# Performance work log

Measured on AMD Instinct MI355X. Metric: run time of the kernel, lower is better.

Reference implementation:

```python
import math
import jax, jax.numpy as jnp
import numpy as np

B, FEAT, H, W = 4, 256, 48, 48
NH = 8
PE = 10            # pe_dim -> 3*PE = 30 positional channels
DK = FEAT // NH    # 32
DV = FEAT // NH    # 32
SCALE = 2.0 * math.pi
TEMPERATURE = 10000.0
BN_EPS = 1e-5


def pos_en_sine(h, w, num_pos_feats=PE):
    """3-axis sine positional encoding (y, x, and a constant 'o' axis) -> [3*PE, h, w]."""
    eps = 1e-6
    ones = jnp.ones((h, w), jnp.float32)
    y_embed = jnp.cumsum(ones, axis=0)
    x_embed = jnp.cumsum(ones, axis=1)
    y_embed = y_embed / (y_embed[-1:, :] + eps) * SCALE
    x_embed = x_embed / (x_embed[:, -1:] + eps) * SCALE
    o_embed = ones * SCALE  # third axis, constant when no explicit pos is given
    dim_t = jnp.arange(num_pos_feats, dtype=jnp.float32)
    dim_t = TEMPERATURE ** (2.0 * jnp.floor(dim_t / 2.0) / num_pos_feats)

    def enc(e):  # e: [h, w] -> [h, w, PE] interleaved sin/cos
        p = e[..., None] / dim_t
        return jnp.stack([jnp.sin(p[..., 0::2]), jnp.cos(p[..., 1::2])], axis=-1).reshape(h, w, num_pos_feats)

    pe = jnp.concatenate([enc(y_embed), enc(x_embed), enc(o_embed)], axis=-1)  # [h, w, 3*PE]
    return jnp.transpose(pe, (2, 0, 1))  # [3*PE, h, w]


def conv1x1(w, x):  # w: [out_c, in_c], x: [b, in_c, h, w]
    return jnp.einsum('oc,bchw->bohw', w, x)


def setup_inputs() -> dict:
    key = jax.random.key(0)
    ks = jax.random.split(key, 16)
    s = 0.02
    return {
        'q': jax.random.normal(ks[0], (B, FEAT, H, W), jnp.float32),
        'k': jax.random.normal(ks[1], (B, FEAT, H, W), jnp.float32),
        'v': jax.random.normal(ks[2], (B, FEAT, H, W), jnp.float32),
        'wq': jax.random.normal(ks[3], (NH * DK, FEAT + 3 * PE), jnp.float32) * s,
        'wk': jax.random.normal(ks[4], (NH * DK, FEAT + 3 * PE), jnp.float32) * s,
        'wv': jax.random.normal(ks[5], (NH * DV, FEAT), jnp.float32) * s,
        'wfc': jax.random.normal(ks[6], (FEAT, NH * DV), jnp.float32) * s,
        'w1': jax.random.normal(ks[7], (FEAT, FEAT), jnp.float32) * s,
        'b1': jnp.zeros((FEAT,), jnp.float32),
        'w2': jax.random.normal(ks[8], (FEAT, FEAT), jnp.float32) * s,
        'b2': jnp.zeros((FEAT,), jnp.float32),
        'gamma': jnp.ones((FEAT,), jnp.float32),
        'beta': jnp.zeros((FEAT,), jnp.float32),
    }


def reference(q, k, v, wq, wk, wv, wfc, w1, b1, w2, b2, gamma, beta):
    b, c, h, w = q.shape
    n = h * w
    pe = pos_en_sine(h, w)                                # [3*PE, h, w]
    peb = jnp.broadcast_to(pe[None], (b,) + pe.shape)
    qc = jnp.concatenate([q, peb], axis=1)                # [b, FEAT+30, h, w]
    kc = jnp.concatenate([k, peb], axis=1)
    # multi-head softmax attention over all spatial tokens
    Q = conv1x1(wq, qc).reshape(b, NH, DK, n)             # [b, nh, dk, n]
    K = conv1x1(wk, kc).reshape(b, NH, DK, n)
    V = conv1x1(wv, v).reshape(b, NH, DV, n)
    scores = jnp.einsum('bhdn,bhdm->bhnm', Q, K) / jnp.sqrt(jnp.float32(DK))
    attn = jax.nn.softmax(scores, axis=-1)                # [b, nh, n, n]
    O = jnp.einsum('bhnm,bhdm->bhdn', attn, V).reshape(b, NH * DV, h, w)
    O = conv1x1(wfc, O)                                   # [b, FEAT, h, w]
    # pointwise FFN + residual
    h1 = jax.nn.relu(conv1x1(w1, O) + b1[None, :, None, None])
    h2 = conv1x1(w2, h1) + b2[None, :, None, None]
    out = O + h2
    # BatchNorm2d (training mode: batch statistics over (b, h, w), biased var)
    mean = jnp.mean(out, axis=(0, 2, 3), keepdims=True)
    var = jnp.var(out, axis=(0, 2, 3), keepdims=True)
    out = (out - mean) / jnp.sqrt(var + BN_EPS)
    out = out * gamma[None, :, None, None] + beta[None, :, None, None]
    return out
```

## Files before the change

kernel.cpp:

```cpp
#include <hip/hip_runtime.h>
#include <hip/hip_bf16.h>

#define NTOK 2304

typedef short  short8  __attribute__((ext_vector_type(8)));
typedef unsigned short ushort8v __attribute__((ext_vector_type(8)));
typedef float  f32x4   __attribute__((ext_vector_type(4)));

static __device__ __forceinline__ unsigned short f2bfu(float f){
  __hip_bfloat16 h = __float2bfloat16(f);
  union { __hip_bfloat16 h; unsigned short u; } cv; cv.h = h; return cv.u;
}
static __device__ __forceinline__ unsigned pack2r(float a, float b){
  unsigned ua = __float_as_uint(a) + 0x8000u;
  unsigned ub = __float_as_uint(b) + 0x8000u;
  return (ua >> 16) | (ub & 0xFFFF0000u);
}


__global__ void trip_kernel(float* out, int n){
  int i = blockIdx.x*256 + threadIdx.x;
  if (i < n) out[i] = 1000.0f;
}

__global__ __launch_bounds__(256) void setup_kernel(
    const float* __restrict__ q, const float* __restrict__ k,
    const float* __restrict__ v,
    const float* __restrict__ wq, const float* __restrict__ wk,
    const float* __restrict__ wv, const float* __restrict__ wfc,
    const float* __restrict__ w1, const float* __restrict__ w2,
    unsigned short* __restrict__ qT, unsigned short* __restrict__ kT,
    unsigned short* __restrict__ vT,
    unsigned short* __restrict__ wqp, unsigned short* __restrict__ wkp,
    unsigned short* __restrict__ wvb, unsigned short* __restrict__ wfcb,
    unsigned short* __restrict__ w1b, unsigned short* __restrict__ w2b,
    float* __restrict__ bns){
  const int bid = blockIdx.x;
  const int t = threadIdx.x;
  __shared__ __align__(16) unsigned short tile[64*72];

  if (bid < 1728){
    if (bid == 0){ bns[t] = 0.f; bns[256+t] = 0.f; }
    const int x = bid % 36, rem = bid / 36;
    const int y = rem % 4, z = rem / 4;
    const int tz = z >> 2, b = z & 3;
    const float* src = (tz==0) ? q : ((tz==1) ? k : v);
    unsigned short* dst = (tz==0) ? qT : ((tz==1) ? kT : vT);
    const int W = (tz==2) ? 256 : 288;
    const int n0 = x*64, c0 = y*64;
    const int jj = t & 7, cl = t >> 3;
    #pragma unroll
    for (int p=0; p<2; p++){
      int c = c0 + 32*p + cl;
      const float* s = src + (size_t)(b*256 + c)*NTOK + n0 + 8*jj;
      float4 f0 = *(const float4*)s;
      float4 f1 = *(const float4*)(s + 4);
      unsigned short* tr = tile + 32*p + cl;
      tr[(8*jj+0)*72] = f2bfu(f0.x); tr[(8*jj+1)*72] = f2bfu(f0.y);
      tr[(8*jj+2)*72] = f2bfu(f0.z); tr[(8*jj+3)*72] = f2bfu(f0.w);
      tr[(8*jj+4)*72] = f2bfu(f1.x); tr[(8*jj+5)*72] = f2bfu(f1.y);
      tr[(8*jj+6)*72] = f2bfu(f1.z); tr[(8*jj+7)*72] = f2bfu(f1.w);
    }
    __syncthreads();
    #pragma unroll
    for (int p=0; p<2; p++){
      int nl = 32*p + cl;
      ushort8v val = *(const ushort8v*)(tile + nl*72 + 8*jj);
      *(ushort8v*)(dst + (size_t)(b*2304 + n0 + nl)*W + c0 + 8*jj) = val;
    }
  } else if (bid < 1800){
    const int id2 = bid - 1728;
    const int x = id2 % 9, yy = id2 / 9;
    const int n = x*256 + t;
    unsigned short* buf = (yy < 4) ? qT : kT;
    const int b = yy & 3;
    const int i = n / 48, j = n - 48*i;
    const float k2pi = 6.283185307179586f;
    const float f = k2pi / 48.000001f;
    float ey = (float)(i+1) * f;
    float ex = (float)(j+1) * f;
    unsigned short u[32];
    #pragma unroll
    for (int p=0; p<10; p++){
      float inv = exp2f(-2.6575424759098898f * (float)(p >> 1));
      float vy = ey*inv, vx = ex*inv, vo = k2pi*inv;
      u[p]    = f2bfu((p&1) ? cosf(vy) : sinf(vy));
      u[10+p] = f2bfu((p&1) ? cosf(vx) : sinf(vx));
      u[20+p] = f2bfu((p&1) ? cosf(vo) : sinf(vo));
    }
    u[30] = 0; u[31] = 0;
    unsigned short* dst = buf + (size_t)(b*2304 + n)*288 + 256;
    #pragma unroll
    for (int m=0; m<4; m++) *(ushort8v*)(dst + 8*m) = *(const ushort8v*)(u + 8*m);
  } else if (bid < 2376){
    const int id3 = bid - 1800;
    const int x = id3 % 288, y = id3 / 288;
    const int idx = x*256 + t;
    const float* src = y ? wk : wq;
    unsigned short* dst = y ? wkp : wqp;
    const float scale = y ? 1.f : 0.17677669529663689f;
    int row = idx / 288, col = idx - row*288;
    dst[idx] = (col < 286) ? f2bfu(src[row*286 + col] * scale) : (unsigned short)0;
  } else {
    const int id4 = bid - 2376;
    const int x = id4 % 256, y = id4 / 256;
    const int idx = x*256 + t;
    const float* src = (y==0)?wv:((y==1)?wfc:((y==2)?w1:w2));
    unsigned short* dst = (y==0)?wvb:((y==1)?wfcb:((y==2)?w1b:w2b));
    dst[idx] = f2bfu(src[idx]);
  }
}

template<int KSTEPS>
static __device__ __forceinline__ void gemm_core(
    const unsigned short* __restrict__ arow,
    const unsigned short* __restrict__ wrow, int wstride, f32x4* acc){
  #pragma unroll
  for (int kk=0; kk<KSTEPS; kk++){
    short8 af = *(const short8*)(arow + 32*kk);
    #pragma unroll
    for (int to=0; to<2; to++){
      short8 bf = *(const short8*)(wrow + (size_t)(16*to)*wstride + 32*kk);
      acc[to] = __builtin_amdgcn_mfma_f32_16x16x32_bf16(af, bf, acc[to], 0,0,0);
    }
  }
}

static __device__ __forceinline__ void epi_tok(
    const f32x4* acc, unsigned short* __restrict__ out_tok,
    int b, int tok, int n0, int lane, int quad, int cc,
    unsigned short* __restrict__ tlw){
  #pragma unroll
  for (int to=0; to<2; to++)
    #pragma unroll
    for (int r=0; r<4; r++)
      tlw[(4*quad + r)*40 + 16*to + cc] = f2bfu(acc[to][r]);
  const int row = lane & 15, ch = lane >> 4;
  ushort8v val = *(const ushort8v*)(tlw + row*40 + 8*ch);
  *(ushort8v*)(out_tok + (size_t)(b*2304 + tok + row)*256 + n0 + 8*ch) = val;
}

static __device__ __forceinline__ void epi_chan(
    const f32x4* acc, unsigned short* __restrict__ out_chan,
    int b, int tok, int n0, int quad, int cc){
  #pragma unroll
  for (int to=0; to<2; to++){
    ushort4 pk;
    pk.x = f2bfu(acc[to][0]); pk.y = f2bfu(acc[to][1]);
    pk.z = f2bfu(acc[to][2]); pk.w = f2bfu(acc[to][3]);
    *(ushort4*)(out_chan + (size_t)(b*256 + n0 + 16*to + cc)*NTOK + tok + 4*quad) = pk;
  }
}

__global__ __launch_bounds__(256) void qkv_kernel(
    const unsigned short* __restrict__ qT, const unsigned short* __restrict__ kT,
    const unsigned short* __restrict__ vT,
    const unsigned short* __restrict__ wqp, const unsigned short* __restrict__ wkp,
    const unsigned short* __restrict__ wvb,
    unsigned short* __restrict__ Qt, unsigned short* __restrict__ Kt,
    unsigned short* __restrict__ V2){
  const int t = threadIdx.x;
  const int w = t >> 6, lane = t & 63;
  const int quad = lane >> 4, cc = lane & 15;
  const int t0 = blockIdx.x*64, n0 = blockIdx.y*32;
  const int tz = blockIdx.z >> 2, b = blockIdx.z & 3;
  const int tok = t0 + 16*w;
  __shared__ __align__(16) unsigned short tl[4*16*40];
  unsigned short* tlw = tl + w*640;

  f32x4 acc[2];
  acc[0] = (f32x4){0.f,0.f,0.f,0.f}; acc[1] = acc[0];

  if (tz == 0){
    const unsigned short* arow = qT + (size_t)(b*2304 + tok + cc)*288 + 8*quad;
    const unsigned short* wrow = wqp + (size_t)(n0 + cc)*288 + 8*quad;
    gemm_core<9>(arow, wrow, 288, acc);
    epi_tok(acc, Qt, b, tok, n0, lane, quad, cc, tlw);
  } else if (tz == 1){
    const unsigned short* arow = kT + (size_t)(b*2304 + tok + cc)*288 + 8*quad;
    const unsigned short* wrow = wkp + (size_t)(n0 + cc)*288 + 8*quad;
    gemm_core<9>(arow, wrow, 288, acc);
    epi_tok(acc, Kt, b, tok, n0, lane, quad, cc, tlw);
  } else {
    const unsigned short* arow = vT + (size_t)(b*2304 + tok + cc)*256 + 8*quad;
    const unsigned short* wrow = wvb + (size_t)(n0 + cc)*256 + 8*quad;
    gemm_core<8>(arow, wrow, 256, acc);
    epi_chan(acc, V2, b, tok, n0, quad, cc);
  }
}

template<int EPI>
__global__ __launch_bounds__(256) void gemm2_kernel(
    const unsigned short* __restrict__ aT,
    const unsigned short* __restrict__ wgt,
    const float* __restrict__ bias,
    unsigned short* __restrict__ out_tok,
    unsigned short* __restrict__ out_chan,
    const unsigned short* __restrict__ resid,
    float* __restrict__ pre_out, float* __restrict__ bns, int relu){
  const int t = threadIdx.x;
  const int w = t >> 6, lane = t & 63;
  const int quad = lane >> 4, cc = lane & 15;
  const int t0 = blockIdx.x*64, n0 = blockIdx.y*32, b = blockIdx.z;
  const int tok = t0 + 16*w;
  __shared__ __align__(16) unsigned short tl[4*16*40];
  unsigned short* tlw = tl + w*640;

  const unsigned short* arow = aT + (size_t)(b*2304 + tok + cc)*256 + 8*quad;
  const unsigned short* wrow = wgt + (size_t)(n0 + cc)*256 + 8*quad;
  f32x4 acc[2];
  acc[0] = (f32x4){0.f,0.f,0.f,0.f}; acc[1] = acc[0];
  gemm_core<8>(arow, wrow, 256, acc);

  if (bias){
    #pragma unroll
    for (int to=0; to<2; to++){
      float bv = bias[n0 + 16*to + cc];
      #pragma unroll
      for (int r=0; r<4; r++) acc[to][r] += bv;
    }
  }
  if (relu){
    #pragma unroll
    for (int to=0; to<2; to++)
      #pragma unroll
      for (int r=0; r<4; r++) acc[to][r] = fmaxf(acc[to][r], 0.f);
  }

  if (EPI == 2){
    epi_chan(acc, out_chan, b, tok, n0, quad, cc);
    epi_tok(acc, out_tok, b, tok, n0, lane, quad, cc, tlw);
  }
  if (EPI == 0){
    epi_tok(acc, out_tok, b, tok, n0, lane, quad, cc, tlw);
  }
  if (EPI == 3){
    #pragma unroll
    for (int to=0; to<2; to++){
      size_t co = (size_t)(b*256 + n0 + 16*to + cc)*NTOK + tok + 4*quad;
      ushort4 rr = *(const ushort4*)(resid + co);
      float p0 = acc[to][0] + __uint_as_float((unsigned)rr.x << 16);
      float p1 = acc[to][1] + __uint_as_float((unsigned)rr.y << 16);
      float p2 = acc[to][2] + __uint_as_float((unsigned)rr.z << 16);
      float p3 = acc[to][3] + __uint_as_float((unsigned)rr.w << 16);
      *(float4*)(pre_out + co) = make_float4(p0,p1,p2,p3);
      float s1 = (p0+p1)+(p2+p3);
      float s2 = (p0*p0+p1*p1)+(p2*p2+p3*p3);
      s1 += __shfl_xor(s1, 16, 64); s1 += __shfl_xor(s1, 32, 64);
      s2 += __shfl_xor(s2, 16, 64); s2 += __shfl_xor(s2, 32, 64);
      if (quad == 0){
        atomicAdd(&bns[n0 + 16*to + cc],       s1);
        atomicAdd(&bns[256 + n0 + 16*to + cc], s2);
      }
    }
  }
}

__global__ __launch_bounds__(256) void attn_kernel(
    const unsigned short* __restrict__ Qt, const unsigned short* __restrict__ Kt,
    const unsigned short* __restrict__ V2, unsigned short* __restrict__ AO){
  const int t = threadIdx.x;
  const int w = t >> 6, lane = t & 63;
  const int quad = lane >> 4, cc = lane & 15;
  const int h = blockIdx.y, b = blockIdx.z;
  const int q0 = blockIdx.x*32;

  const unsigned short* qb = Qt + (size_t)(b*2304 + q0 + cc)*256 + h*32 + 8*quad;
  short8 qf0 = *(const short8*)(qb);
  short8 qf1 = *(const short8*)(qb + 16*256);

  const unsigned short* kb = Kt + (size_t)(b*2304 + cc)*256 + h*32 + 8*quad;
  const unsigned short* vb = V2 + (size_t)(b*256 + h*32 + cc)*NTOK + 8*quad;

  __shared__ __align__(16) unsigned short attn_lds[10240];
  unsigned short* Pl = attn_lds + w*2560;

  f32x4 o00 = {0.f,0.f,0.f,0.f}, o10 = o00, o01 = o00, o11 = o00;
  float lsum0 = 0.f, lsum1 = 0.f;

  const int kstart = w*576, kend = kstart + 576;
  short8 kf0 = *(const short8*)(kb + (size_t)kstart*256);
  short8 kf1 = *(const short8*)(kb + (size_t)(kstart+16)*256);
  short8 vf0 = *(const short8*)(vb + kstart);
  short8 vf1 = *(const short8*)(vb + (size_t)16*NTOK + kstart);

  #pragma unroll 1
  for (int k0 = kstart; k0 < kend; k0 += 32){
    int kn = (k0 + 32 < kend) ? k0 + 32 : kstart;
    short8 nk0 = *(const short8*)(kb + (size_t)kn*256);
    short8 nk1 = *(const short8*)(kb + (size_t)(kn+16)*256);
    short8 nv0 = *(const short8*)(vb + kn);
    short8 nv1 = *(const short8*)(vb + (size_t)16*NTOK + kn);

    f32x4 z = {0.f,0.f,0.f,0.f};
    f32x4 s00 = __builtin_amdgcn_mfma_f32_16x16x32_bf16(kf0, qf0, z, 0,0,0);
    f32x4 s10 = __builtin_amdgcn_mfma_f32_16x16x32_bf16(kf1, qf0, z, 0,0,0);
    f32x4 s01 = __builtin_amdgcn_mfma_f32_16x16x32_bf16(kf0, qf1, z, 0,0,0);
    f32x4 s11 = __builtin_amdgcn_mfma_f32_16x16x32_bf16(kf1, qf1, z, 0,0,0);

    #pragma unroll
    for (int r=0; r<4; r++){
      s00[r] = __expf(s00[r]); s10[r] = __expf(s10[r]);
      s01[r] = __expf(s01[r]); s11[r] = __expf(s11[r]);
    }
    lsum0 += ((s00[0]+s00[1])+(s00[2]+s00[3])) + ((s10[0]+s10[1])+(s10[2]+s10[3]));
    lsum1 += ((s01[0]+s01[1])+(s01[2]+s01[3])) + ((s11[0]+s11[1])+(s11[2]+s11[3]));

    { uint2 pw; pw.x = pack2r(s00[0],s00[1]); pw.y = pack2r(s00[2],s00[3]);
      *(uint2*)(Pl + cc*40 + 4*quad) = pw; }
    { uint2 pw; pw.x = pack2r(s10[0],s10[1]); pw.y = pack2r(s10[2],s10[3]);
      *(uint2*)(Pl + cc*40 + 16 + 4*quad) = pw; }
    { uint2 pw; pw.x = pack2r(s01[0],s01[1]); pw.y = pack2r(s01[2],s01[3]);
      *(uint2*)(Pl + (16+cc)*40 + 4*quad) = pw; }
    { uint2 pw; pw.x = pack2r(s11[0],s11[1]); pw.y = pack2r(s11[2],s11[3]);
      *(uint2*)(Pl + (16+cc)*40 + 16 + 4*quad) = pw; }

    short8 pf0 = *(const short8*)(Pl + cc*40 + 8*quad);
    short8 pf1 = *(const short8*)(Pl + (16+cc)*40 + 8*quad);

    o00 = __builtin_amdgcn_mfma_f32_16x16x32_bf16(vf0, pf0, o00, 0,0,0);
    o10 = __builtin_amdgcn_mfma_f32_16x16x32_bf16(vf1, pf0, o10, 0,0,0);
    o01 = __builtin_amdgcn_mfma_f32_16x16x32_bf16(vf0, pf1, o01, 0,0,0);
    o11 = __builtin_amdgcn_mfma_f32_16x16x32_bf16(vf1, pf1, o11, 0,0,0);

    kf0 = nk0; kf1 = nk1; vf0 = nv0; vf1 = nv1;
  }

  lsum0 += __shfl_xor(lsum0, 16, 64); lsum0 += __shfl_xor(lsum0, 32, 64);
  lsum1 += __shfl_xor(lsum1, 16, 64); lsum1 += __shfl_xor(lsum1, 32, 64);

  float* mg = (float*)(attn_lds + w*2560);
  {
    const int base = lane*17;
    #pragma unroll
    for (int i=0;i<4;i++){
      mg[base + i]      = o00[i];
      mg[base + 4 + i]  = o10[i];
      mg[base + 8 + i]  = o01[i];
      mg[base + 12 + i] = o11[i];
    }
    mg[1088 + lane] = lsum0;
    mg[1152 + lane] = lsum1;
  }
  __syncthreads();

  const float* m0 = (const float*)(attn_lds);
  const float* m1 = (const float*)(attn_lds + 2560);
  const float* m2 = (const float*)(attn_lds + 5120);
  const float* m3 = (const float*)(attn_lds + 7680);
  float ls0 = (m0[1088+lane]+m1[1088+lane]) + (m2[1088+lane]+m3[1088+lane]);
  float ls1 = (m0[1152+lane]+m1[1152+lane]) + (m2[1152+lane]+m3[1152+lane]);
  float inv = 1.f / ((w & 2) ? ls1 : ls0);

  const int off = lane*17 + w*4;
  float r0 = (m0[off+0]+m1[off+0]) + (m2[off+0]+m3[off+0]);
  float r1 = (m0[off+1]+m1[off+1]) + (m2[off+1]+m3[off+1]);
  float r2 = (m0[off+2]+m1[off+2]) + (m2[off+2]+m3[off+2]);
  float r3 = (m0[off+3]+m1[off+3]) + (m2[off+3]+m3[off+3]);

  const int qcol = q0 + ((w & 2) ? 16 : 0) + cc;
  const int dofs = (w & 1) ? 16 : 0;
  ushort4 pk;
  pk.x = f2bfu(r0*inv); pk.y = f2bfu(r1*inv);
  pk.z = f2bfu(r2*inv); pk.w = f2bfu(r3*inv);
  *(ushort4*)(AO + (size_t)(b*2304 + qcol)*256 + h*32 + dofs + 4*quad) = pk;
}

__global__ __launch_bounds__(256) void bn_final_kernel(
    const float* __restrict__ pre, const float* __restrict__ bns,
    const float* __restrict__ g, const float* __restrict__ bt,
    float* __restrict__ out){
  int i0 = (blockIdx.x*256 + threadIdx.x)*4;
  int ch = (i0 / NTOK) & 255;
  float mean = bns[ch] * (1.f/9216.f);
  float var  = bns[256+ch] * (1.f/9216.f) - mean*mean;
  float scl = g[ch] * rsqrtf(fmaxf(var, 0.f) + 1e-5f);
  float sh  = bt[ch] - mean*scl;
  float4 x = *(const float4*)(pre + i0);
  *(float4*)(out + i0) = make_float4(x.x*scl+sh, x.y*scl+sh, x.z*scl+sh, x.w*scl+sh);
}

extern "C" void kernel_launch(void* const* d_in, const int* in_sizes, int n_in,
                              void* d_out, int out_size, void* d_ws, size_t ws_size,
                              hipStream_t stream){
  const size_t NEED = 2112 + (size_t)15155200*2;
  if (ws_size < NEED){
    trip_kernel<<<dim3((out_size+255)/256), dim3(256), 0, stream>>>((float*)d_out, out_size);
    return;
  }
  const float* q   = (const float*)d_in[0];
  const float* k   = (const float*)d_in[1];
  const float* v   = (const float*)d_in[2];
  const float* wq  = (const float*)d_in[3];
  const float* wk  = (const float*)d_in[4];
  const float* wv  = (const float*)d_in[5];
  const float* wfc = (const float*)d_in[6];
  const float* w1  = (const float*)d_in[7];
  const float* b1  = (const float*)d_in[8];
  const float* w2  = (const float*)d_in[9];
  const float* b2  = (const float*)d_in[10];
  const float* gm  = (const float*)d_in[11];
  const float* bt  = (const float*)d_in[12];

  float* ws  = (float*)d_ws;
  float* bns = ws;
  unsigned short* ub = (unsigned short*)(ws + 528);
  unsigned short* u_qT = ub;
  unsigned short* u_kT = ub + 2654208;
  unsigned short* u_vT = ub + 5308416;
  unsigned short* u_Qt = ub + 7667712;
  unsigned short* u_Kt = ub + 10027008;
  unsigned short* u_V2 = ub + 12386304;
  unsigned short* wqp  = ub + 14745600;
  unsigned short* wkp  = ub + 14819328;
  unsigned short* wvb  = ub + 14893056;
  unsigned short* wfcb = ub + 14958592;
  unsigned short* w1b  = ub + 15024128;
  unsigned short* w2b  = ub + 15089664;
  unsigned short* AO  = u_qT;
  unsigned short* h1  = u_kT;
  unsigned short* Ofc = u_vT;
  unsigned short* Oc  = u_Qt;
  float* pre = (float*)(u_Kt);

  setup_kernel<<<dim3(3400), dim3(256), 0, stream>>>(
      q, k, v, wq, wk, wv, wfc, w1, w2,
      u_qT, u_kT, u_vT, wqp, wkp, wvb, wfcb, w1b, w2b, bns);

  qkv_kernel<<<dim3(36,8,12), dim3(256), 0, stream>>>(u_qT, u_kT, u_vT, wqp, wkp, wvb, u_Qt, u_Kt, u_V2);

  attn_kernel<<<dim3(72,8,4), dim3(256), 0, stream>>>(u_Qt, u_Kt, u_V2, AO);

  gemm2_kernel<2><<<dim3(36,8,4), dim3(256), 0, stream>>>(AO,  wfcb, nullptr, Ofc, Oc, nullptr, nullptr, nullptr, 0);
  gemm2_kernel<0><<<dim3(36,8,4), dim3(256), 0, stream>>>(Ofc, w1b,  b1,      h1,  nullptr, nullptr, nullptr, nullptr, 1);
  gemm2_kernel<3><<<dim3(36,8,4), dim3(256), 0, stream>>>(h1,  w2b,  b2,      nullptr, nullptr, Oc, pre, bns, 0);

  bn_final_kernel<<<dim3(2304), dim3(256), 0, stream>>>(pre, bns, gm, bt, (float*)d_out);
}
```

Before: 272.5 us.

## Keep softmax probabilities in registers for PV MFMA and fold log2e into Wk

The attention loop no longer writes exp scores to LDS and reads them back. The P operand for the PV MFMA is packed directly from the score accumulator registers, and the V loads are permuted into two 4-element halves so the k-index ordering matches the register layout. log2(e) is folded into the K weight conversion so the raw exp2 instruction can replace __expf. The cost is narrower 8-byte V loads in place of 16-byte loads, and a rounding change from scaling the weights before the bf16 conversion.

```diff
diff --git a/kernel.cpp b/kernel.cpp
--- a/kernel.cpp
+++ b/kernel.cpp
@@ -4,6 +4,7 @@
 #define NTOK 2304
 
 typedef short  short8  __attribute__((ext_vector_type(8)));
+typedef short  short4v __attribute__((ext_vector_type(4)));
 typedef unsigned short ushort8v __attribute__((ext_vector_type(8)));
 typedef float  f32x4   __attribute__((ext_vector_type(4)));
 
@@ -98,7 +99,7 @@
     const int idx = x*256 + t;
     const float* src = y ? wk : wq;
     unsigned short* dst = y ? wkp : wqp;
-    const float scale = y ? 1.f : 0.17677669529663689f;
+    const float scale = y ? 1.4426950408889634f : 0.17677669529663689f;
     int row = idx / 288, col = idx - row*288;
     dst[idx] = (col < 286) ? f2bfu(src[row*286 + col] * scale) : (unsigned short)0;
   } else {
@@ -270,10 +271,10 @@
   short8 qf1 = *(const short8*)(qb + 16*256);
 
   const unsigned short* kb = Kt + (size_t)(b*2304 + cc)*256 + h*32 + 8*quad;
-  const unsigned short* vb = V2 + (size_t)(b*256 + h*32 + cc)*NTOK + 8*quad;
+  const unsigned short* vb0 = V2 + (size_t)(b*256 + h*32 + cc)*NTOK;
+  const unsigned short* vb1 = vb0 + (size_t)16*NTOK;
 
   __shared__ __align__(16) unsigned short attn_lds[10240];
-  unsigned short* Pl = attn_lds + w*2560;
 
   f32x4 o00 = {0.f,0.f,0.f,0.f}, o10 = o00, o01 = o00, o11 = o00;
   float lsum0 = 0.f, lsum1 = 0.f;
@@ -281,16 +282,20 @@
   const int kstart = w*576, kend = kstart + 576;
   short8 kf0 = *(const short8*)(kb + (size_t)kstart*256);
   short8 kf1 = *(const short8*)(kb + (size_t)(kstart+16)*256);
-  short8 vf0 = *(const short8*)(vb + kstart);
-  short8 vf1 = *(const short8*)(vb + (size_t)16*NTOK + kstart);
+  short4v v0lo = *(const short4v*)(vb0 + kstart + 4*quad);
+  short4v v0hi = *(const short4v*)(vb0 + kstart + 16 + 4*quad);
+  short4v v1lo = *(const short4v*)(vb1 + kstart + 4*quad);
+  short4v v1hi = *(const short4v*)(vb1 + kstart + 16 + 4*quad);
 
   #pragma unroll 1
   for (int k0 = kstart; k0 < kend; k0 += 32){
     int kn = (k0 + 32 < kend) ? k0 + 32 : kstart;
     short8 nk0 = *(const short8*)(kb + (size_t)kn*256);
     short8 nk1 = *(const short8*)(kb + (size_t)(kn+16)*256);
-    short8 nv0 = *(const short8*)(vb + kn);
-    short8 nv1 = *(const short8*)(vb + (size_t)16*NTOK + kn);
+    short4v n0lo = *(const short4v*)(vb0 + kn + 4*quad);
+    short4v n0hi = *(const short4v*)(vb0 + kn + 16 + 4*quad);
+    short4v n1lo = *(const short4v*)(vb1 + kn + 4*quad);
+    short4v n1hi = *(const short4v*)(vb1 + kn + 16 + 4*quad);
 
     f32x4 z = {0.f,0.f,0.f,0.f};
     f32x4 s00 = __builtin_amdgcn_mfma_f32_16x16x32_bf16(kf0, qf0, z, 0,0,0);
@@ -300,30 +305,31 @@
 
     #pragma unroll
     for (int r=0; r<4; r++){
-      s00[r] = __expf(s00[r]); s10[r] = __expf(s10[r]);
-      s01[r] = __expf(s01[r]); s11[r] = __expf(s11[r]);
+      s00[r] = __builtin_amdgcn_exp2f(s00[r]);
+      s10[r] = __builtin_amdgcn_exp2f(s10[r]);
+      s01[r] = __builtin_amdgcn_exp2f(s01[r]);
+      s11[r] = __builtin_amdgcn_exp2f(s11[r]);
     }
     lsum0 += ((s00[0]+s00[1])+(s00[2]+s00[3])) + ((s10[0]+s10[1])+(s10[2]+s10[3]));
     lsum1 += ((s01[0]+s01[1])+(s01[2]+s01[3])) + ((s11[0]+s11[1])+(s11[2]+s11[3]));
 
-    { uint2 pw; pw.x = pack2r(s00[0],s00[1]); pw.y = pack2r(s00[2],s00[3]);
-      *(uint2*)(Pl + cc*40 + 4*quad) = pw; }
-    { uint2 pw; pw.x = pack2r(s10[0],s10[1]); pw.y = pack2r(s10[2],s10[3]);
-      *(uint2*)(Pl + cc*40 + 16 + 4*quad) = pw; }
-    { uint2 pw; pw.x = pack2r(s01[0],s01[1]); pw.y = pack2r(s01[2],s01[3]);
-      *(uint2*)(Pl + (16+cc)*40 + 4*quad) = pw; }
-    { uint2 pw; pw.x = pack2r(s11[0],s11[1]); pw.y = pack2r(s11[2],s11[3]);
-      *(uint2*)(Pl + (16+cc)*40 + 16 + 4*quad) = pw; }
-
-    short8 pf0 = *(const short8*)(Pl + cc*40 + 8*quad);
-    short8 pf1 = *(const short8*)(Pl + (16+cc)*40 + 8*quad);
-
-    o00 = __builtin_amdgcn_mfma_f32_16x16x32_bf16(vf0, pf0, o00, 0,0,0);
-    o10 = __builtin_amdgcn_mfma_f32_16x16x32_bf16(vf1, pf0, o10, 0,0,0);
-    o01 = __builtin_amdgcn_mfma_f32_16x16x32_bf16(vf0, pf1, o01, 0,0,0);
-    o11 = __builtin_amdgcn_mfma_f32_16x16x32_bf16(vf1, pf1, o11, 0,0,0);
-
-    kf0 = nk0; kf1 = nk1; vf0 = nv0; vf1 = nv1;
+    union { unsigned u[4]; short8 s; } pf0u, pf1u;
+    pf0u.u[0] = pack2r(s00[0], s00[1]); pf0u.u[1] = pack2r(s00[2], s00[3]);
+    pf0u.u[2] = pack2r(s10[0], s10[1]); pf0u.u[3] = pack2r(s10[2], s10[3]);
+    pf1u.u[0] = pack2r(s01[0], s01[1]); pf1u.u[1] = pack2r(s01[2], s01[3]);
+    pf1u.u[2] = pack2r(s11[0], s11[1]); pf1u.u[3] = pack2r(s11[2], s11[3]);
+
+    union { short4v h[2]; short8 s; } vf0u, vf1u;
+    vf0u.h[0] = v0lo; vf0u.h[1] = v0hi;
+    vf1u.h[0] = v1lo; vf1u.h[1] = v1hi;
+
+    o00 = __builtin_amdgcn_mfma_f32_16x16x32_bf16(vf0u.s, pf0u.s, o00, 0,0,0);
+    o10 = __builtin_amdgcn_mfma_f32_16x16x32_bf16(vf1u.s, pf0u.s, o10, 0,0,0);
+    o01 = __builtin_amdgcn_mfma_f32_16x16x32_bf16(vf0u.s, pf1u.s, o01, 0,0,0);
+    o11 = __builtin_amdgcn_mfma_f32_16x16x32_bf16(vf1u.s, pf1u.s, o11, 0,0,0);
+
+    kf0 = nk0; kf1 = nk1;
+    v0lo = n0lo; v0hi = n0hi; v1lo = n1lo; v1hi = n1hi;
   }
 
   lsum0 += __shfl_xor(lsum0, 16, 64); lsum0 += __shfl_xor(lsum0, 32, 64);
```

Measured after the change: 302.1 us. 10.9% more time.
